# Performance work log

Hardware: AMD Instinct MI355X
Metric: run time of the kernel (lower is better)

Reference implementation:

```python
import jax, jax.numpy as jnp
import numpy as np
import math

D_MODEL = 1024
N_HEADS = 16
D_K = D_MODEL // N_HEADS
B, T = 4, 2048


def setup_inputs() -> dict:
    key = jax.random.key(0)
    k1, k2, k3, k4, k5 = jax.random.split(key, 5)
    s = 1.0 / math.sqrt(D_MODEL)
    return {
        "x": jax.random.normal(k1, (B, T, D_MODEL), dtype=jnp.float32),
        "W_qkv": jax.random.normal(k2, (D_MODEL, 3 * D_MODEL), dtype=jnp.float32) * s,
        "b_qkv": jax.random.normal(k3, (3 * D_MODEL,), dtype=jnp.float32) * 0.02,
        "W_proj": jax.random.normal(k4, (D_MODEL, D_MODEL), dtype=jnp.float32) * s,
        "b_proj": jax.random.normal(k5, (D_MODEL,), dtype=jnp.float32) * 0.02,
    }


def reference(x, W_qkv, b_qkv, W_proj, b_proj):
    Bsz, Tlen, C = x.shape
    qkv = x @ W_qkv + b_qkv                       # [B,T,3C]
    q, k, v = jnp.split(qkv, 3, axis=2)
    # [B,T,C] -> [B,H,T,dk]
    def heads(t):
        return t.reshape(Bsz, Tlen, N_HEADS, D_K).transpose(0, 2, 1, 3)
    q, k, v = heads(q), heads(k), heads(v)
    att = jnp.einsum("bhqd,bhkd->bhqk", q, k) * (1.0 / math.sqrt(D_K))
    causal = jnp.tril(jnp.ones((Tlen, Tlen), dtype=bool))
    att = jnp.where(causal, att, -jnp.inf)
    att = jax.nn.softmax(att, axis=-1)
    y = jnp.einsum("bhqk,bhkd->bhqd", att, v)     # [B,H,T,dk]
    y = y.transpose(0, 2, 1, 3).reshape(Bsz, Tlen, C)
    return y @ W_proj + b_proj
```

## Files before the change

### kernel.cpp

```cpp
#include <hip/hip_runtime.h>
#include <math.h>
#include <stdint.h>

#define D_MODEL 1024
#define NH      16
#define DK      64
#define BS      4
#define TS      2048
#define M_ROWS  (BS*TS)
#define C3      (3*D_MODEL)

typedef __attribute__((ext_vector_type(8))) short          short8;
typedef __attribute__((ext_vector_type(4))) float          f32x4;
typedef __attribute__((ext_vector_type(8))) __bf16         bf16x8;
typedef __attribute__((ext_vector_type(4))) unsigned short ushort4_t;

static __device__ __forceinline__ unsigned short f2bf(float f) {
    unsigned u = __builtin_bit_cast(unsigned, f);
    u += 0x7fffu + ((u >> 16) & 1u);
    return (unsigned short)(u >> 16);
}
static __device__ __forceinline__ float bf2f(unsigned short h) {
    unsigned u = ((unsigned)h) << 16;
    return __builtin_bit_cast(float, u);
}
static __device__ __forceinline__ f32x4 mfma16(short8 a, short8 b, f32x4 c) {
    return __builtin_amdgcn_mfma_f32_16x16x32_bf16(
        __builtin_bit_cast(bf16x8, a), __builtin_bit_cast(bf16x8, b), c, 0, 0, 0);
}
static __device__ __forceinline__ void gll16(const void* g, void* l) {
    __builtin_amdgcn_global_load_lds(
        (const __attribute__((address_space(1))) void*)g,
        (__attribute__((address_space(3))) void*)l, 16, 0, 0);
}

__global__ __launch_bounds__(256)
void cast_split(const float* __restrict__ src, unsigned short* __restrict__ hi,
                unsigned short* __restrict__ lo, int n4) {
    int i = blockIdx.x * blockDim.x + threadIdx.x;
    const int stride = gridDim.x * blockDim.x;
    for (; i < n4; i += stride) {
        float4 v = reinterpret_cast<const float4*>(src)[i];
        float f0 = v.x, f1 = v.y, f2 = v.z, f3 = v.w;
        ushort4_t h, l;
        h[0] = f2bf(f0); l[0] = f2bf(f0 - bf2f(h[0]));
        h[1] = f2bf(f1); l[1] = f2bf(f1 - bf2f(h[1]));
        h[2] = f2bf(f2); l[2] = f2bf(f2 - bf2f(h[2]));
        h[3] = f2bf(f3); l[3] = f2bf(f3 - bf2f(h[3]));
        reinterpret_cast<ushort4_t*>(hi)[i] = h;
        reinterpret_cast<ushort4_t*>(lo)[i] = l;
    }
}

__global__ __launch_bounds__(256)
void cast_wT(const float* __restrict__ W, unsigned short* __restrict__ Th,
             unsigned short* __restrict__ Tl, int K, int N) {
    __shared__ float Ls[32][36];
    const int tid = threadIdx.x;
    const int n0 = blockIdx.x * 32, k0 = blockIdx.y * 32;
    {
        const int row = tid >> 3, c4 = tid & 7;
        float4 v = *reinterpret_cast<const float4*>(&W[(size_t)(k0 + row) * N + n0 + c4 * 4]);
        *reinterpret_cast<float4*>(&Ls[row][c4 * 4]) = v;
    }
    __syncthreads();
    {
        const int nl = tid >> 3, c4 = tid & 7;
        ushort4_t h, l;
#pragma unroll
        for (int j = 0; j < 4; ++j) {
            float f = Ls[c4 * 4 + j][nl];
            h[j] = f2bf(f);
            l[j] = f2bf(f - bf2f(h[j]));
        }
        const size_t o = (size_t)(n0 + nl) * K + k0 + c4 * 4;
        *reinterpret_cast<ushort4_t*>(&Th[o]) = h;
        *reinterpret_cast<ushort4_t*>(&Tl[o]) = l;
    }
}

__global__ __launch_bounds__(256)
void v_transpose(const unsigned short* __restrict__ qh, const unsigned short* __restrict__ ql,
                 unsigned short* __restrict__ vth, unsigned short* __restrict__ vtl) {
    __shared__ unsigned short Ls[64][68];
    const int tt = blockIdx.x, bh = blockIdx.y;
    const int b = bh >> 4, h = bh & 15;
    const size_t src_base = ((size_t)b * TS + (size_t)tt * 64) * C3 + 2 * D_MODEL + h * DK;
    const size_t dst_base = (size_t)bh * DK * TS + (size_t)tt * 64;
#pragma unroll
    for (int pass = 0; pass < 2; ++pass) {
        const unsigned short* src = pass ? ql : qh;
        unsigned short* dst = pass ? vtl : vth;
        if (pass) __syncthreads();
        for (int c = threadIdx.x; c < 1024; c += 256) {
            const int t = c >> 4, c4 = c & 15;
            ushort4_t v = *reinterpret_cast<const ushort4_t*>(&src[src_base + (size_t)t * C3 + c4 * 4]);
            *reinterpret_cast<ushort4_t*>(&Ls[t][c4 * 4]) = v;
        }
        __syncthreads();
        for (int c = threadIdx.x; c < 1024; c += 256) {
            const int d = c >> 4, t4 = c & 15;
            ushort4_t o;
            o[0] = Ls[t4 * 4 + 0][d];
            o[1] = Ls[t4 * 4 + 1][d];
            o[2] = Ls[t4 * 4 + 2][d];
            o[3] = Ls[t4 * 4 + 3][d];
            *reinterpret_cast<ushort4_t*>(&dst[dst_base + (size_t)d * TS + t4 * 4]) = o;
        }
    }
}

template <int BF16OUT>
__global__ __launch_bounds__(256)
void gemm_split(const unsigned short* __restrict__ Ah_g, const unsigned short* __restrict__ Al_g,
                const unsigned short* __restrict__ Bh_g, const unsigned short* __restrict__ Bl_g,
                const float* __restrict__ bias,
                float* __restrict__ Cf, unsigned short* __restrict__ Ch,
                unsigned short* __restrict__ Cl,
                int M, int N, int K) {
    __shared__ unsigned short AhL[128 * 32];
    __shared__ unsigned short AlL[128 * 32];
    __shared__ unsigned short BhL[128 * 32];
    __shared__ unsigned short BlL[128 * 32];

    const int tid  = threadIdx.x;
    const int lane = tid & 63, wid = tid >> 6;
    const int wm = wid >> 1, wn = wid & 1;
    const int bm = blockIdx.y * 128, bn = blockIdx.x * 128;
    const int lr = lane & 15, kg = lane >> 4;

    f32x4 acc[4][4];
#pragma unroll
    for (int m = 0; m < 4; ++m)
#pragma unroll
        for (int n = 0; n < 4; ++n) acc[m][n] = (f32x4){0.f, 0.f, 0.f, 0.f};

    for (int k0 = 0; k0 < K; k0 += 32) {
        __syncthreads();
#pragma unroll
        for (int j = 0; j < 2; ++j) {
            const int si  = j * 256 + wid * 64 + lane;
            const int row = si >> 2, cc = si & 3;
            const int sc  = cc ^ ((row >> 1) & 3);
            const int lo  = (j * 256 + wid * 64) * 8;
            const size_t ga = (size_t)(bm + row) * K + k0 + sc * 8;
            const size_t gb = (size_t)(bn + row) * K + k0 + sc * 8;
            gll16(&Ah_g[ga], &AhL[lo]);
            gll16(&Al_g[ga], &AlL[lo]);
            gll16(&Bh_g[gb], &BhL[lo]);
            gll16(&Bl_g[gb], &BlL[lo]);
        }
        __syncthreads();

        short8 ah[4], al[4], bh[4], bl[4];
#pragma unroll
        for (int m = 0; m < 4; ++m) {
            const int r = wm * 64 + m * 16 + lr;
            const int s = kg ^ ((r >> 1) & 3);
            ah[m] = *reinterpret_cast<const short8*>(&AhL[r * 32 + s * 8]);
            al[m] = *reinterpret_cast<const short8*>(&AlL[r * 32 + s * 8]);
        }
#pragma unroll
        for (int n = 0; n < 4; ++n) {
            const int r = wn * 64 + n * 16 + lr;
            const int s = kg ^ ((r >> 1) & 3);
            bh[n] = *reinterpret_cast<const short8*>(&BhL[r * 32 + s * 8]);
            bl[n] = *reinterpret_cast<const short8*>(&BlL[r * 32 + s * 8]);
        }
#pragma unroll
        for (int m = 0; m < 4; ++m)
#pragma unroll
            for (int n = 0; n < 4; ++n) {
                acc[m][n] = mfma16(ah[m], bh[n], acc[m][n]);
                acc[m][n] = mfma16(ah[m], bl[n], acc[m][n]);
                acc[m][n] = mfma16(al[m], bh[n], acc[m][n]);
            }
    }

    const int og = lane >> 4, oc = lane & 15;
#pragma unroll
    for (int n = 0; n < 4; ++n) {
        const int gc = bn + wn * 64 + n * 16 + oc;
        const float bz = bias[gc];
#pragma unroll
        for (int m = 0; m < 4; ++m) {
            const int gr0 = bm + wm * 64 + m * 16 + og * 4;
#pragma unroll
            for (int rr = 0; rr < 4; ++rr) {
                const float v = acc[m][n][rr] + bz;
                const size_t idx = (size_t)(gr0 + rr) * N + gc;
                if (BF16OUT) {
                    const unsigned short hh = f2bf(v);
                    Ch[idx] = hh;
                    Cl[idx] = f2bf(v - bf2f(hh));
                } else {
                    Cf[idx] = v;
                }
            }
        }
    }
}

__global__ __launch_bounds__(512, 2)
void attn_mfma(const unsigned short* __restrict__ qkvh,
               const unsigned short* __restrict__ vth, const unsigned short* __restrict__ vtl,
               unsigned short* __restrict__ yh, unsigned short* __restrict__ yl) {
    const int pr = blockIdx.x;
    const int bh = blockIdx.y;
    const int b = bh >> 4, h = bh & 15;
    const int tid = threadIdx.x, w = tid >> 6, lane = tid & 63;
    const int lr = lane & 15, lg = lane >> 4;

    __shared__ unsigned short Kt[2][64 * 64];
    __shared__ unsigned short Vhs[2][64 * 64];
    __shared__ unsigned short Vls[2][64 * 64];
    __shared__ unsigned short Ps[8][32 * 64];

    const size_t kbase  = (size_t)b * TS * C3 + D_MODEL + (size_t)h * DK;
    const size_t vbase  = (size_t)bh * DK * TS;
    const size_t qbase  = (size_t)b * TS * C3 + (size_t)h * DK;
    unsigned short* PsW = &Ps[w][0];

    const f32x4 fz = (f32x4){0.f, 0.f, 0.f, 0.f};

    const int srow = tid >> 3;
    const int ssc  = (tid & 7) ^ (srow & 7);
    const int slds = (w * 64) * 8;

    for (int qi = 0; qi < 2; ++qi) {
        const int qt = qi ? (7 - pr) : pr;
        const int q0 = qt * 256;
        const int qwbase = q0 + w * 32;

        short8 qreg[2][2];
#pragma unroll
        for (int mf = 0; mf < 2; ++mf) {
            const size_t qrow = qbase + (size_t)(qwbase + mf * 16 + lr) * C3;
            qreg[mf][0] = *reinterpret_cast<const short8*>(&qkvh[qrow + lg * 8]);
            qreg[mf][1] = *reinterpret_cast<const short8*>(&qkvh[qrow + 32 + lg * 8]);
        }

        f32x4 yacc[4][2];
#pragma unroll
        for (int df = 0; df < 4; ++df)
#pragma unroll
            for (int qf = 0; qf < 2; ++qf) yacc[df][qf] = fz;
        float mrun[2], lrun[2];
#pragma unroll
        for (int qf = 0; qf < 2; ++qf) { mrun[qf] = -1e30f; lrun[qf] = 0.f; }

        const int nkt = 4 * qt + 4;
        int cur = 0;

        auto stage = [&](int buf, int kt) {
            gll16(&qkvh[kbase + (size_t)(kt * 64 + srow) * C3 + ssc * 8], &Kt[buf][slds]);
            gll16(&vth[vbase + (size_t)srow * TS + kt * 64 + ssc * 8], &Vhs[buf][slds]);
            gll16(&vtl[vbase + (size_t)srow * TS + kt * 64 + ssc * 8], &Vls[buf][slds]);
        };
        auto ldsf = [&](const unsigned short* Tt, int row, int kslot) -> short8 {
            return *reinterpret_cast<const short8*>(
                reinterpret_cast<const char*>(Tt) + row * 128 + (((kslot ^ (row & 7)) & 7) << 4));
        };

        stage(cur, 0);
        for (int kt = 0; kt < nkt; ++kt) {
            __syncthreads();
            if (kt + 1 < nkt) stage(cur ^ 1, kt + 1);

            if (kt * 64 <= qwbase + 31) {
                f32x4 s[2][4];
                __builtin_amdgcn_s_setprio(1);
#pragma unroll
                for (int nf = 0; nf < 4; ++nf) {
                    const int krow = nf * 16 + lr;
                    short8 ka0 = ldsf(Kt[cur], krow, lg);
                    short8 ka1 = ldsf(Kt[cur], krow, 4 + lg);
#pragma unroll
                    for (int mf = 0; mf < 2; ++mf)
                        s[mf][nf] = mfma16(ka1, qreg[mf][1], mfma16(ka0, qreg[mf][0], fz));
                }
                __builtin_amdgcn_s_setprio(0);
#pragma unroll
                for (int mf = 0; mf < 2; ++mf)
#pragma unroll
                    for (int nf = 0; nf < 4; ++nf) s[mf][nf] *= 0.125f;
                if (kt * 64 + 63 > qwbase) {
#pragma unroll
                    for (int mf = 0; mf < 2; ++mf) {
                        const int q = qwbase + mf * 16 + lr;
#pragma unroll
                        for (int nf = 0; nf < 4; ++nf)
#pragma unroll
                            for (int rr = 0; rr < 4; ++rr)
                                if (kt * 64 + nf * 16 + lg * 4 + rr > q) s[mf][nf][rr] = -1e30f;
                    }
                }
                float sclv[2];
#pragma unroll
                for (int mf = 0; mf < 2; ++mf) {
                    float rm = s[mf][0][0];
#pragma unroll
                    for (int nf = 0; nf < 4; ++nf)
#pragma unroll
                        for (int rr = 0; rr < 4; ++rr) rm = fmaxf(rm, s[mf][nf][rr]);
                    rm = fmaxf(rm, __shfl_xor(rm, 16, 64));
                    rm = fmaxf(rm, __shfl_xor(rm, 32, 64));
                    const float mn = fmaxf(mrun[mf], rm);
                    float rs = 0.f;
#pragma unroll
                    for (int nf = 0; nf < 4; ++nf)
#pragma unroll
                        for (int rr = 0; rr < 4; ++rr) {
                            const float p = __expf(s[mf][nf][rr] - mn);
                            s[mf][nf][rr] = p;
                            rs += p;
                        }
                    rs += __shfl_xor(rs, 16, 64);
                    rs += __shfl_xor(rs, 32, 64);
                    sclv[mf] = __expf(mrun[mf] - mn);
                    lrun[mf] = lrun[mf] * sclv[mf] + rs;
                    mrun[mf] = mn;
                }
#pragma unroll
                for (int df = 0; df < 4; ++df)
#pragma unroll
                    for (int qf = 0; qf < 2; ++qf) yacc[df][qf] *= sclv[qf];
#pragma unroll
                for (int mf = 0; mf < 2; ++mf) {
                    const int q = mf * 16 + lr;
#pragma unroll
                    for (int nf = 0; nf < 4; ++nf) {
                        ushort4_t pw;
                        pw[0] = f2bf(s[mf][nf][0]);
                        pw[1] = f2bf(s[mf][nf][1]);
                        pw[2] = f2bf(s[mf][nf][2]);
                        pw[3] = f2bf(s[mf][nf][3]);
                        *reinterpret_cast<ushort4_t*>(
                            reinterpret_cast<char*>(PsW) +
                            ((q * 128 + (nf * 16 + lg * 4) * 2) ^ ((q & 7) << 4))) = pw;
                    }
                }
#pragma unroll
                for (int kf = 0; kf < 2; ++kf) {
                    short8 pb[2];
#pragma unroll
                    for (int qf = 0; qf < 2; ++qf) {
                        const int q = qf * 16 + lr;
                        pb[qf] = *reinterpret_cast<const short8*>(
                            reinterpret_cast<const char*>(PsW) +
                            q * 128 + ((((kf << 2) + lg) ^ (q & 7)) << 4));
                    }
                    __builtin_amdgcn_s_setprio(1);
#pragma unroll
                    for (int df = 0; df < 4; ++df) {
                        const int d = df * 16 + lr;
                        short8 va = ldsf(Vhs[cur], d, (kf << 2) + lg);
                        short8 vb = ldsf(Vls[cur], d, (kf << 2) + lg);
#pragma unroll
                        for (int qf = 0; qf < 2; ++qf) {
                            yacc[df][qf] = mfma16(va, pb[qf], yacc[df][qf]);
                            yacc[df][qf] = mfma16(vb, pb[qf], yacc[df][qf]);
                        }
                    }
                    __builtin_amdgcn_s_setprio(0);
                }
            }
            cur ^= 1;
        }

#pragma unroll
        for (int qf = 0; qf < 2; ++qf) {
            const float inv = 1.f / lrun[qf];
            const size_t ro = ((size_t)b * TS + (qwbase + qf * 16 + lr)) * D_MODEL + h * DK;
#pragma unroll
            for (int df = 0; df < 4; ++df) {
                ushort4_t oh, ol;
#pragma unroll
                for (int rr = 0; rr < 4; ++rr) {
                    const float v = yacc[df][qf][rr] * inv;
                    oh[rr] = f2bf(v);
                    ol[rr] = f2bf(v - bf2f(oh[rr]));
                }
                *reinterpret_cast<ushort4_t*>(&yh[ro + df * 16 + lg * 4]) = oh;
                *reinterpret_cast<ushort4_t*>(&yl[ro + df * 16 + lg * 4]) = ol;
            }
        }
    }
}

extern "C" void kernel_launch(void* const* d_in, const int* in_sizes, int n_in,
                              void* d_out, int out_size, void* d_ws, size_t ws_size,
                              hipStream_t stream) {
    const float* x      = (const float*)d_in[0];
    const float* W_qkv  = (const float*)d_in[1];
    const float* b_qkv  = (const float*)d_in[2];
    const float* W_proj = (const float*)d_in[3];
    const float* b_proj = (const float*)d_in[4];
    float* out = (float*)d_out;

    char* ws = (char*)d_ws;
    size_t off = 0;
    auto carve = [&](size_t elems) {
        unsigned short* p = (unsigned short*)(ws + off);
        off += elems * sizeof(unsigned short);
        return p;
    };
    unsigned short* xh   = carve((size_t)M_ROWS * D_MODEL);
    unsigned short* xl   = carve((size_t)M_ROWS * D_MODEL);
    unsigned short* wqh  = carve((size_t)C3 * D_MODEL);
    unsigned short* wql  = carve((size_t)C3 * D_MODEL);
    unsigned short* wph  = carve((size_t)D_MODEL * D_MODEL);
    unsigned short* wpl  = carve((size_t)D_MODEL * D_MODEL);
    unsigned short* qkvh = carve((size_t)M_ROWS * C3);
    unsigned short* qkvl = carve((size_t)M_ROWS * C3);
    unsigned short* vth  = carve((size_t)BS * NH * DK * TS);
    unsigned short* vtl  = carve((size_t)BS * NH * DK * TS);
    unsigned short* yhh  = carve((size_t)M_ROWS * D_MODEL);
    unsigned short* yll  = carve((size_t)M_ROWS * D_MODEL);

    cast_split<<<2048, 256, 0, stream>>>(x, xh, xl, M_ROWS * D_MODEL / 4);
    cast_wT<<<dim3(C3 / 32, D_MODEL / 32), 256, 0, stream>>>(W_qkv, wqh, wql, D_MODEL, C3);
    cast_wT<<<dim3(D_MODEL / 32, D_MODEL / 32), 256, 0, stream>>>(W_proj, wph, wpl, D_MODEL, D_MODEL);

    gemm_split<1><<<dim3(C3 / 128, M_ROWS / 128), 256, 0, stream>>>(
        xh, xl, wqh, wql, b_qkv, nullptr, qkvh, qkvl, M_ROWS, C3, D_MODEL);

    v_transpose<<<dim3(TS / 64, BS * NH), 256, 0, stream>>>(qkvh, qkvl, vth, vtl);

    attn_mfma<<<dim3(4, BS * NH), 512, 0, stream>>>(qkvh, vth, vtl, yhh, yll);

    gemm_split<0><<<dim3(D_MODEL / 128, M_ROWS / 128), 256, 0, stream>>>(
        yhh, yll, wph, wpl, b_proj, out, nullptr, nullptr, M_ROWS, D_MODEL, D_MODEL);
}
```

Baseline: 451.8 us.

## Rewrite split-bf16 GEMM as 256x128 triple-buffered 8-wave pipelined kernel

Replaces the 128x128, 4-wave split-bf16 GEMM with a 256x128 tile run by 8 waves. The three hi/lo product terms are folded into a single virtual K axis of length 3K. Global-to-LDS loads go into a three-stage ring buffer with explicit vmcnt waits, barriers and s_setprio, so loads for tile t+2 overlap the MFMAs for tile t. The goal is to hide memory latency and cut per-iteration synchronisation. In exchange it uses more LDS (one block per CU), adds complex index math, and makes correctness depend on the hand-placed waitcnt and barrier schedule.

```diff
diff --git a/kernel.cpp b/kernel.cpp
--- a/kernel.cpp
+++ b/kernel.cpp
@@ -111,23 +111,22 @@
 }
 
 template <int BF16OUT>
-__global__ __launch_bounds__(256)
-void gemm_split(const unsigned short* __restrict__ Ah_g, const unsigned short* __restrict__ Al_g,
-                const unsigned short* __restrict__ Bh_g, const unsigned short* __restrict__ Bl_g,
-                const float* __restrict__ bias,
-                float* __restrict__ Cf, unsigned short* __restrict__ Ch,
-                unsigned short* __restrict__ Cl,
-                int M, int N, int K) {
-    __shared__ unsigned short AhL[128 * 32];
-    __shared__ unsigned short AlL[128 * 32];
-    __shared__ unsigned short BhL[128 * 32];
-    __shared__ unsigned short BlL[128 * 32];
+__global__ __launch_bounds__(512, 1)
+void gemm_split_8ph(const unsigned short* __restrict__ Ah_g, const unsigned short* __restrict__ Al_g,
+                    const unsigned short* __restrict__ Bh_g, const unsigned short* __restrict__ Bl_g,
+                    const float* __restrict__ bias,
+                    float* __restrict__ Cf, unsigned short* __restrict__ Ch,
+                    unsigned short* __restrict__ Cl,
+                    int M, int N, int K) {
+    __shared__ unsigned short ALs[3][256 * 64];
+    __shared__ unsigned short BLs[3][128 * 64];
 
     const int tid  = threadIdx.x;
     const int lane = tid & 63, wid = tid >> 6;
     const int wm = wid >> 1, wn = wid & 1;
-    const int bm = blockIdx.y * 128, bn = blockIdx.x * 128;
+    const int bm = blockIdx.y * 256, bn = blockIdx.x * 128;
     const int lr = lane & 15, kg = lane >> 4;
+    const int NT = (3 * K) / 64;
 
     f32x4 acc[4][4];
 #pragma unroll
@@ -135,46 +134,102 @@
 #pragma unroll
         for (int n = 0; n < 4; ++n) acc[m][n] = (f32x4){0.f, 0.f, 0.f, 0.f};
 
-    for (int k0 = 0; k0 < K; k0 += 32) {
-        __syncthreads();
+    auto stageA = [&](int t) {
+        const int b3 = t % 3;
+#pragma unroll
+        for (int half = 0; half < 2; ++half)
+#pragma unroll
+            for (int j = 0; j < 2; ++j) {
+                const int L   = (wid * 2 + j) * 64 + lane;
+                const int row = L >> 3, sl = L & 7;
+                const int sv  = sl ^ (row & 7);
+                const int vc  = t * 2 + (sv >> 2);
+                const int r3  = vc % 3;
+                const int c   = vc / 3;
+                const unsigned short* pl = (r3 == 2) ? Al_g : Ah_g;
+                const size_t ga = (size_t)(bm + half * 128 + row) * K + c * 32 + (sv & 3) * 8;
+                gll16(&pl[ga], &ALs[b3][half * 8192 + (wid * 2 + j) * 512]);
+            }
+    };
+    auto stageB = [&](int t) {
+        const int b3 = t % 3;
 #pragma unroll
         for (int j = 0; j < 2; ++j) {
-            const int si  = j * 256 + wid * 64 + lane;
-            const int row = si >> 2, cc = si & 3;
-            const int sc  = cc ^ ((row >> 1) & 3);
-            const int lo  = (j * 256 + wid * 64) * 8;
-            const size_t ga = (size_t)(bm + row) * K + k0 + sc * 8;
-            const size_t gb = (size_t)(bn + row) * K + k0 + sc * 8;
-            gll16(&Ah_g[ga], &AhL[lo]);
-            gll16(&Al_g[ga], &AlL[lo]);
-            gll16(&Bh_g[gb], &BhL[lo]);
-            gll16(&Bl_g[gb], &BlL[lo]);
-        }
-        __syncthreads();
-
-        short8 ah[4], al[4], bh[4], bl[4];
-#pragma unroll
-        for (int m = 0; m < 4; ++m) {
-            const int r = wm * 64 + m * 16 + lr;
-            const int s = kg ^ ((r >> 1) & 3);
-            ah[m] = *reinterpret_cast<const short8*>(&AhL[r * 32 + s * 8]);
-            al[m] = *reinterpret_cast<const short8*>(&AlL[r * 32 + s * 8]);
-        }
+            const int L   = (wid * 2 + j) * 64 + lane;
+            const int row = L >> 3, sl = L & 7;
+            const int sv  = sl ^ (row & 7);
+            const int vc  = t * 2 + (sv >> 2);
+            const int r3  = vc % 3;
+            const int c   = vc / 3;
+            const unsigned short* pl = (r3 == 1) ? Bl_g : Bh_g;
+            const size_t gb = (size_t)(bn + row) * K + c * 32 + (sv & 3) * 8;
+            gll16(&pl[gb], &BLs[b3][(wid * 2 + j) * 512]);
+        }
+    };
+    auto rdA = [&](int cur, int m, int kf) -> short8 {
+        const int row = wm * 64 + m * 16 + lr;
+        const int sp  = (kf * 4 + kg) ^ (row & 7);
+        return *reinterpret_cast<const short8*>(&ALs[cur][row * 64 + sp * 8]);
+    };
+    auto rdB = [&](int cur, int n, int kf) -> short8 {
+        const int row = wn * 64 + n * 16 + lr;
+        const int sp  = (kf * 4 + kg) ^ (row & 7);
+        return *reinterpret_cast<const short8*>(&BLs[cur][row * 64 + sp * 8]);
+    };
+
+    stageA(0); stageB(0);
+    stageA(1); stageB(1);
+    asm volatile("s_waitcnt vmcnt(6)" ::: "memory");
+    __builtin_amdgcn_s_barrier();
+
+    for (int t = 0; t < NT; ++t) {
+        const int cur = t % 3;
+        short8 bfr[4][2];
 #pragma unroll
         for (int n = 0; n < 4; ++n) {
-            const int r = wn * 64 + n * 16 + lr;
-            const int s = kg ^ ((r >> 1) & 3);
-            bh[n] = *reinterpret_cast<const short8*>(&BhL[r * 32 + s * 8]);
-            bl[n] = *reinterpret_cast<const short8*>(&BlL[r * 32 + s * 8]);
-        }
-#pragma unroll
-        for (int m = 0; m < 4; ++m)
+            bfr[n][0] = rdB(cur, n, 0);
+            bfr[n][1] = rdB(cur, n, 1);
+        }
+        short8 afr[2][2];
+#pragma unroll
+        for (int m = 0; m < 2; ++m) {
+            afr[m][0] = rdA(cur, m, 0);
+            afr[m][1] = rdA(cur, m, 1);
+        }
+        if (t + 2 < NT) stageA(t + 2);
+        __builtin_amdgcn_s_barrier();
+        __builtin_amdgcn_s_setprio(1);
+#pragma unroll
+        for (int m = 0; m < 2; ++m)
 #pragma unroll
             for (int n = 0; n < 4; ++n) {
-                acc[m][n] = mfma16(ah[m], bh[n], acc[m][n]);
-                acc[m][n] = mfma16(ah[m], bl[n], acc[m][n]);
-                acc[m][n] = mfma16(al[m], bh[n], acc[m][n]);
-            }
+                acc[m][n] = mfma16(afr[m][0], bfr[n][0], acc[m][n]);
+                acc[m][n] = mfma16(afr[m][1], bfr[n][1], acc[m][n]);
+            }
+        __builtin_amdgcn_s_setprio(0);
+        __builtin_amdgcn_s_barrier();
+#pragma unroll
+        for (int m = 0; m < 2; ++m) {
+            afr[m][0] = rdA(cur, m + 2, 0);
+            afr[m][1] = rdA(cur, m + 2, 1);
+        }
+        if (t + 2 < NT) {
+            stageB(t + 2);
+            asm volatile("s_waitcnt vmcnt(6)" ::: "memory");
+        } else if (t + 1 < NT) {
+            asm volatile("s_waitcnt vmcnt(0)" ::: "memory");
+        }
+        __builtin_amdgcn_s_barrier();
+        __builtin_amdgcn_s_setprio(1);
+#pragma unroll
+        for (int m = 0; m < 2; ++m)
+#pragma unroll
+            for (int n = 0; n < 4; ++n) {
+                acc[m + 2][n] = mfma16(afr[m][0], bfr[n][0], acc[m + 2][n]);
+                acc[m + 2][n] = mfma16(afr[m][1], bfr[n][1], acc[m + 2][n]);
+            }
+        __builtin_amdgcn_s_setprio(0);
+        __builtin_amdgcn_s_barrier();
     }
 
     const int og = lane >> 4, oc = lane & 15;
@@ -422,13 +477,13 @@
     cast_wT<<<dim3(C3 / 32, D_MODEL / 32), 256, 0, stream>>>(W_qkv, wqh, wql, D_MODEL, C3);
     cast_wT<<<dim3(D_MODEL / 32, D_MODEL / 32), 256, 0, stream>>>(W_proj, wph, wpl, D_MODEL, D_MODEL);
 
-    gemm_split<1><<<dim3(C3 / 128, M_ROWS / 128), 256, 0, stream>>>(
+    gemm_split_8ph<1><<<dim3(C3 / 128, M_ROWS / 256), 512, 0, stream>>>(
         xh, xl, wqh, wql, b_qkv, nullptr, qkvh, qkvl, M_ROWS, C3, D_MODEL);
 
     v_transpose<<<dim3(TS / 64, BS * NH), 256, 0, stream>>>(qkvh, qkvl, vth, vtl);
 
     attn_mfma<<<dim3(4, BS * NH), 512, 0, stream>>>(qkvh, vth, vtl, yhh, yll);
 
-    gemm_split<0><<<dim3(D_MODEL / 128, M_ROWS / 128), 256, 0, stream>>>(
+    gemm_split_8ph<0><<<dim3(D_MODEL / 128, M_ROWS / 256), 512, 0, stream>>>(
         yhh, yll, wph, wpl, b_proj, out, nullptr, nullptr, M_ROWS, D_MODEL, D_MODEL);
 }
```

Measured after the change: 508.5 us. +12.5%, slower.

## Rewrite split-bf16 GEMM as persistent 256x128 tiles with double-buffered LDS

Applied to the files above, without the earlier changes.

Replaces the 128x128 single-buffered GEMM with a 512-thread kernel that computes 256x128 tiles, launched as exactly 256 blocks, one per CU, each looping over NTILE column tiles. The block index is remapped so blocks sharing A rows group together for L2 reuse. The next K-slice is loaded into a second LDS buffer while the current one feeds the MFMAs, with s_setprio raised around the MFMA section. The aim is to hide global-load latency, halve barriers per K-step and fill the machine evenly, at the cost of more LDS use and one block per CU, which gives less latency hiding across blocks. The tile mapping hard-codes K=1024 (32 steps) and grid dimensions specific to these shapes.

```diff
diff --git a/kernel.cpp b/kernel.cpp
--- a/kernel.cpp
+++ b/kernel.cpp
@@ -110,91 +110,112 @@
     }
 }
 
-template <int BF16OUT>
-__global__ __launch_bounds__(256)
-void gemm_split(const unsigned short* __restrict__ Ah_g, const unsigned short* __restrict__ Al_g,
-                const unsigned short* __restrict__ Bh_g, const unsigned short* __restrict__ Bl_g,
-                const float* __restrict__ bias,
-                float* __restrict__ Cf, unsigned short* __restrict__ Ch,
-                unsigned short* __restrict__ Cl,
-                int M, int N, int K) {
-    __shared__ unsigned short AhL[128 * 32];
-    __shared__ unsigned short AlL[128 * 32];
-    __shared__ unsigned short BhL[128 * 32];
-    __shared__ unsigned short BlL[128 * 32];
+template <int BF16OUT, int NTILE>
+__global__ __launch_bounds__(512, 1)
+void gemm_split2(const unsigned short* __restrict__ Ah_g, const unsigned short* __restrict__ Al_g,
+                 const unsigned short* __restrict__ Bh_g, const unsigned short* __restrict__ Bl_g,
+                 const float* __restrict__ bias,
+                 float* __restrict__ Cf, unsigned short* __restrict__ Ch,
+                 unsigned short* __restrict__ Cl,
+                 int M, int N, int K) {
+    __shared__ unsigned short AhL[2][256 * 32];
+    __shared__ unsigned short AlL[2][256 * 32];
+    __shared__ unsigned short BhL[2][128 * 32];
+    __shared__ unsigned short BlL[2][128 * 32];
 
     const int tid  = threadIdx.x;
     const int lane = tid & 63, wid = tid >> 6;
     const int wm = wid >> 1, wn = wid & 1;
-    const int bm = blockIdx.y * 128, bn = blockIdx.x * 128;
     const int lr = lane & 15, kg = lane >> 4;
 
-    f32x4 acc[4][4];
-#pragma unroll
-    for (int m = 0; m < 4; ++m)
-#pragma unroll
-        for (int n = 0; n < 4; ++n) acc[m][n] = (f32x4){0.f, 0.f, 0.f, 0.f};
-
-    for (int k0 = 0; k0 < K; k0 += 32) {
+    const int bid = blockIdx.x;
+    const int mb  = 4 * (bid & 7) + (bid >> 6);
+    const int ng  = (bid >> 3) & 7;
+    const int bm  = mb * 256;
+
+    const int arow0 = tid >> 2;
+    const int ao0   = (tid & 3) ^ ((arow0 >> 1) & 3);
+    const int arow1 = arow0 + 128;
+    const int ao1   = (tid & 3) ^ ((arow1 >> 1) & 3);
+    const int brow  = tid >> 2;
+    const int bo    = (tid & 3) ^ ((brow >> 1) & 3);
+    const int ldsw  = wid * 512;
+
+    for (int it = 0; it < NTILE; ++it) {
+        const int bn = (ng * NTILE + it) * 128;
+
+        f32x4 acc[4][4];
+#pragma unroll
+        for (int m = 0; m < 4; ++m)
+#pragma unroll
+            for (int n = 0; n < 4; ++n) acc[m][n] = (f32x4){0.f, 0.f, 0.f, 0.f};
+
+        auto stage = [&](int buf, int k0) {
+            gll16(&Ah_g[(size_t)(bm + arow0) * K + k0 + ao0 * 8], &AhL[buf][ldsw]);
+            gll16(&Ah_g[(size_t)(bm + arow1) * K + k0 + ao1 * 8], &AhL[buf][4096 + ldsw]);
+            gll16(&Al_g[(size_t)(bm + arow0) * K + k0 + ao0 * 8], &AlL[buf][ldsw]);
+            gll16(&Al_g[(size_t)(bm + arow1) * K + k0 + ao1 * 8], &AlL[buf][4096 + ldsw]);
+            gll16(&Bh_g[(size_t)(bn + brow) * K + k0 + bo * 8], &BhL[buf][ldsw]);
+            gll16(&Bl_g[(size_t)(bn + brow) * K + k0 + bo * 8], &BlL[buf][ldsw]);
+        };
+        auto rd = [&](const unsigned short* P, int r) -> short8 {
+            const int s = kg ^ ((r >> 1) & 3);
+            return *reinterpret_cast<const short8*>(&P[r * 32 + s * 8]);
+        };
+
+        int cur = 0;
+        stage(0, 0);
         __syncthreads();
-#pragma unroll
-        for (int j = 0; j < 2; ++j) {
-            const int si  = j * 256 + wid * 64 + lane;
-            const int row = si >> 2, cc = si & 3;
-            const int sc  = cc ^ ((row >> 1) & 3);
-            const int lo  = (j * 256 + wid * 64) * 8;
-            const size_t ga = (size_t)(bm + row) * K + k0 + sc * 8;
-            const size_t gb = (size_t)(bn + row) * K + k0 + sc * 8;
-            gll16(&Ah_g[ga], &AhL[lo]);
-            gll16(&Al_g[ga], &AlL[lo]);
-            gll16(&Bh_g[gb], &BhL[lo]);
-            gll16(&Bl_g[gb], &BlL[lo]);
-        }
-        __syncthreads();
-
-        short8 ah[4], al[4], bh[4], bl[4];
-#pragma unroll
-        for (int m = 0; m < 4; ++m) {
-            const int r = wm * 64 + m * 16 + lr;
-            const int s = kg ^ ((r >> 1) & 3);
-            ah[m] = *reinterpret_cast<const short8*>(&AhL[r * 32 + s * 8]);
-            al[m] = *reinterpret_cast<const short8*>(&AlL[r * 32 + s * 8]);
-        }
+
+        for (int t = 0; t < 32; ++t) {
+            if (t + 1 < 32) stage(cur ^ 1, (t + 1) * 32);
+
+            short8 ah[4], al[4], bhf[4], blf[4];
+#pragma unroll
+            for (int m = 0; m < 4; ++m) {
+                const int r = wm * 64 + m * 16 + lr;
+                ah[m] = rd(&AhL[cur][0], r);
+                al[m] = rd(&AlL[cur][0], r);
+            }
+#pragma unroll
+            for (int n = 0; n < 4; ++n) {
+                const int r = wn * 64 + n * 16 + lr;
+                bhf[n] = rd(&BhL[cur][0], r);
+                blf[n] = rd(&BlL[cur][0], r);
+            }
+            __builtin_amdgcn_s_setprio(1);
+#pragma unroll
+            for (int m = 0; m < 4; ++m)
+#pragma unroll
+                for (int n = 0; n < 4; ++n) {
+                    acc[m][n] = mfma16(ah[m], bhf[n], acc[m][n]);
+                    acc[m][n] = mfma16(ah[m], blf[n], acc[m][n]);
+                    acc[m][n] = mfma16(al[m], bhf[n], acc[m][n]);
+                }
+            __builtin_amdgcn_s_setprio(0);
+            __syncthreads();
+            cur ^= 1;
+        }
+
+        const int og = lane >> 4, oc = lane & 15;
 #pragma unroll
         for (int n = 0; n < 4; ++n) {
-            const int r = wn * 64 + n * 16 + lr;
-            const int s = kg ^ ((r >> 1) & 3);
-            bh[n] = *reinterpret_cast<const short8*>(&BhL[r * 32 + s * 8]);
-            bl[n] = *reinterpret_cast<const short8*>(&BlL[r * 32 + s * 8]);
-        }
-#pragma unroll
-        for (int m = 0; m < 4; ++m)
-#pragma unroll
-            for (int n = 0; n < 4; ++n) {
-                acc[m][n] = mfma16(ah[m], bh[n], acc[m][n]);
-                acc[m][n] = mfma16(ah[m], bl[n], acc[m][n]);
-                acc[m][n] = mfma16(al[m], bh[n], acc[m][n]);
-            }
-    }
-
-    const int og = lane >> 4, oc = lane & 15;
-#pragma unroll
-    for (int n = 0; n < 4; ++n) {
-        const int gc = bn + wn * 64 + n * 16 + oc;
-        const float bz = bias[gc];
-#pragma unroll
-        for (int m = 0; m < 4; ++m) {
-            const int gr0 = bm + wm * 64 + m * 16 + og * 4;
-#pragma unroll
-            for (int rr = 0; rr < 4; ++rr) {
-                const float v = acc[m][n][rr] + bz;
-                const size_t idx = (size_t)(gr0 + rr) * N + gc;
-                if (BF16OUT) {
-                    const unsigned short hh = f2bf(v);
-                    Ch[idx] = hh;
-                    Cl[idx] = f2bf(v - bf2f(hh));
-                } else {
-                    Cf[idx] = v;
+            const int gc = bn + wn * 64 + n * 16 + oc;
+            const float bz = bias[gc];
+#pragma unroll
+            for (int m = 0; m < 4; ++m) {
+                const int gr0 = bm + wm * 64 + m * 16 + og * 4;
+#pragma unroll
+                for (int rr = 0; rr < 4; ++rr) {
+                    const float v = acc[m][n][rr] + bz;
+                    const size_t idx = (size_t)(gr0 + rr) * N + gc;
+                    if (BF16OUT) {
+                        const unsigned short hh = f2bf(v);
+                        Ch[idx] = hh;
+                        Cl[idx] = f2bf(v - bf2f(hh));
+                    } else {
+                        Cf[idx] = v;
+                    }
                 }
             }
         }
@@ -422,13 +443,13 @@
     cast_wT<<<dim3(C3 / 32, D_MODEL / 32), 256, 0, stream>>>(W_qkv, wqh, wql, D_MODEL, C3);
     cast_wT<<<dim3(D_MODEL / 32, D_MODEL / 32), 256, 0, stream>>>(W_proj, wph, wpl, D_MODEL, D_MODEL);
 
-    gemm_split<1><<<dim3(C3 / 128, M_ROWS / 128), 256, 0, stream>>>(
+    gemm_split2<1, 3><<<256, 512, 0, stream>>>(
         xh, xl, wqh, wql, b_qkv, nullptr, qkvh, qkvl, M_ROWS, C3, D_MODEL);
 
     v_transpose<<<dim3(TS / 64, BS * NH), 256, 0, stream>>>(qkvh, qkvl, vth, vtl);
 
     attn_mfma<<<dim3(4, BS * NH), 512, 0, stream>>>(qkvh, vth, vtl, yhh, yll);
 
-    gemm_split<0><<<dim3(D_MODEL / 128, M_ROWS / 128), 256, 0, stream>>>(
+    gemm_split2<0, 1><<<256, 512, 0, stream>>>(
         yhh, yll, wph, wpl, b_proj, out, nullptr, nullptr, M_ROWS, D_MODEL, D_MODEL);
 }
```

Measured after the change: 458.5 us. About the same (+1.5%).

## Fuse V transpose into QKV GEMM epilogue and give each attention block one query tile

Applied to the files above, without the earlier changes.

The QKV GEMM epilogue now writes the V columns straight into the transposed hi/lo V buffers, so the separate v_transpose kernel and its extra read/write pass over V are gone. The attention kernel no longer pairs a short and a long causal query tile per block. It launches 8 blocks per head, each handling one query tile, which doubles the grid but leaves blocks with uneven causal work. The transposed V stores are 4-element ushort4 writes strided by the sequence length, which may coalesce less well than the old transpose kernel's writes.

```diff
diff --git a/kernel.cpp b/kernel.cpp
--- a/kernel.cpp
+++ b/kernel.cpp
@@ -79,44 +79,14 @@
     }
 }
 
-__global__ __launch_bounds__(256)
-void v_transpose(const unsigned short* __restrict__ qh, const unsigned short* __restrict__ ql,
-                 unsigned short* __restrict__ vth, unsigned short* __restrict__ vtl) {
-    __shared__ unsigned short Ls[64][68];
-    const int tt = blockIdx.x, bh = blockIdx.y;
-    const int b = bh >> 4, h = bh & 15;
-    const size_t src_base = ((size_t)b * TS + (size_t)tt * 64) * C3 + 2 * D_MODEL + h * DK;
-    const size_t dst_base = (size_t)bh * DK * TS + (size_t)tt * 64;
-#pragma unroll
-    for (int pass = 0; pass < 2; ++pass) {
-        const unsigned short* src = pass ? ql : qh;
-        unsigned short* dst = pass ? vtl : vth;
-        if (pass) __syncthreads();
-        for (int c = threadIdx.x; c < 1024; c += 256) {
-            const int t = c >> 4, c4 = c & 15;
-            ushort4_t v = *reinterpret_cast<const ushort4_t*>(&src[src_base + (size_t)t * C3 + c4 * 4]);
-            *reinterpret_cast<ushort4_t*>(&Ls[t][c4 * 4]) = v;
-        }
-        __syncthreads();
-        for (int c = threadIdx.x; c < 1024; c += 256) {
-            const int d = c >> 4, t4 = c & 15;
-            ushort4_t o;
-            o[0] = Ls[t4 * 4 + 0][d];
-            o[1] = Ls[t4 * 4 + 1][d];
-            o[2] = Ls[t4 * 4 + 2][d];
-            o[3] = Ls[t4 * 4 + 3][d];
-            *reinterpret_cast<ushort4_t*>(&dst[dst_base + (size_t)d * TS + t4 * 4]) = o;
-        }
-    }
-}
-
-template <int BF16OUT>
+template <int MODE>
 __global__ __launch_bounds__(256)
 void gemm_split(const unsigned short* __restrict__ Ah_g, const unsigned short* __restrict__ Al_g,
                 const unsigned short* __restrict__ Bh_g, const unsigned short* __restrict__ Bl_g,
                 const float* __restrict__ bias,
                 float* __restrict__ Cf, unsigned short* __restrict__ Ch,
                 unsigned short* __restrict__ Cl,
+                unsigned short* __restrict__ vth, unsigned short* __restrict__ vtl,
                 int M, int N, int K) {
     __shared__ unsigned short AhL[128 * 32];
     __shared__ unsigned short AlL[128 * 32];
@@ -178,23 +148,48 @@
     }
 
     const int og = lane >> 4, oc = lane & 15;
-#pragma unroll
-    for (int n = 0; n < 4; ++n) {
-        const int gc = bn + wn * 64 + n * 16 + oc;
-        const float bz = bias[gc];
-#pragma unroll
-        for (int m = 0; m < 4; ++m) {
-            const int gr0 = bm + wm * 64 + m * 16 + og * 4;
-#pragma unroll
-            for (int rr = 0; rr < 4; ++rr) {
-                const float v = acc[m][n][rr] + bz;
-                const size_t idx = (size_t)(gr0 + rr) * N + gc;
-                if (BF16OUT) {
-                    const unsigned short hh = f2bf(v);
-                    Ch[idx] = hh;
-                    Cl[idx] = f2bf(v - bf2f(hh));
-                } else {
-                    Cf[idx] = v;
+    if (MODE == 2 && bn >= 2048) {
+#pragma unroll
+        for (int n = 0; n < 4; ++n) {
+            const int gc = bn + wn * 64 + n * 16 + oc;
+            const float bz = bias[gc];
+            const int vb  = gc - 2048;
+            const int hh_ = vb >> 6, dd = vb & 63;
+#pragma unroll
+            for (int m = 0; m < 4; ++m) {
+                const int gr0 = bm + wm * 64 + m * 16 + og * 4;
+                ushort4_t vh4, vl4;
+#pragma unroll
+                for (int rr = 0; rr < 4; ++rr) {
+                    const float v = acc[m][n][rr] + bz;
+                    vh4[rr] = f2bf(v);
+                    vl4[rr] = f2bf(v - bf2f(vh4[rr]));
+                }
+                const size_t o = ((size_t)((gr0 >> 11) * 16 + hh_) * 64 + dd) * 2048
+                               + (size_t)(gr0 & 2047);
+                *reinterpret_cast<ushort4_t*>(&vth[o]) = vh4;
+                *reinterpret_cast<ushort4_t*>(&vtl[o]) = vl4;
+            }
+        }
+    } else {
+#pragma unroll
+        for (int n = 0; n < 4; ++n) {
+            const int gc = bn + wn * 64 + n * 16 + oc;
+            const float bz = bias[gc];
+#pragma unroll
+            for (int m = 0; m < 4; ++m) {
+                const int gr0 = bm + wm * 64 + m * 16 + og * 4;
+#pragma unroll
+                for (int rr = 0; rr < 4; ++rr) {
+                    const float v = acc[m][n][rr] + bz;
+                    const size_t idx = (size_t)(gr0 + rr) * N + gc;
+                    if (MODE >= 1) {
+                        const unsigned short hh = f2bf(v);
+                        Ch[idx] = hh;
+                        Cl[idx] = f2bf(v - bf2f(hh));
+                    } else {
+                        Cf[idx] = v;
+                    }
                 }
             }
         }
@@ -205,7 +200,7 @@
 void attn_mfma(const unsigned short* __restrict__ qkvh,
                const unsigned short* __restrict__ vth, const unsigned short* __restrict__ vtl,
                unsigned short* __restrict__ yh, unsigned short* __restrict__ yl) {
-    const int pr = blockIdx.x;
+    const int qt = blockIdx.x;
     const int bh = blockIdx.y;
     const int b = bh >> 4, h = bh & 15;
     const int tid = threadIdx.x, w = tid >> 6, lane = tid & 63;
@@ -227,163 +222,159 @@
     const int ssc  = (tid & 7) ^ (srow & 7);
     const int slds = (w * 64) * 8;
 
-    for (int qi = 0; qi < 2; ++qi) {
-        const int qt = qi ? (7 - pr) : pr;
-        const int q0 = qt * 256;
-        const int qwbase = q0 + w * 32;
-
-        short8 qreg[2][2];
-#pragma unroll
-        for (int mf = 0; mf < 2; ++mf) {
-            const size_t qrow = qbase + (size_t)(qwbase + mf * 16 + lr) * C3;
-            qreg[mf][0] = *reinterpret_cast<const short8*>(&qkvh[qrow + lg * 8]);
-            qreg[mf][1] = *reinterpret_cast<const short8*>(&qkvh[qrow + 32 + lg * 8]);
-        }
-
-        f32x4 yacc[4][2];
-#pragma unroll
-        for (int df = 0; df < 4; ++df)
-#pragma unroll
-            for (int qf = 0; qf < 2; ++qf) yacc[df][qf] = fz;
-        float mrun[2], lrun[2];
-#pragma unroll
-        for (int qf = 0; qf < 2; ++qf) { mrun[qf] = -1e30f; lrun[qf] = 0.f; }
-
-        const int nkt = 4 * qt + 4;
-        int cur = 0;
-
-        auto stage = [&](int buf, int kt) {
-            gll16(&qkvh[kbase + (size_t)(kt * 64 + srow) * C3 + ssc * 8], &Kt[buf][slds]);
-            gll16(&vth[vbase + (size_t)srow * TS + kt * 64 + ssc * 8], &Vhs[buf][slds]);
-            gll16(&vtl[vbase + (size_t)srow * TS + kt * 64 + ssc * 8], &Vls[buf][slds]);
-        };
-        auto ldsf = [&](const unsigned short* Tt, int row, int kslot) -> short8 {
-            return *reinterpret_cast<const short8*>(
-                reinterpret_cast<const char*>(Tt) + row * 128 + (((kslot ^ (row & 7)) & 7) << 4));
-        };
-
-        stage(cur, 0);
-        for (int kt = 0; kt < nkt; ++kt) {
-            __syncthreads();
-            if (kt + 1 < nkt) stage(cur ^ 1, kt + 1);
-
-            if (kt * 64 <= qwbase + 31) {
-                f32x4 s[2][4];
+    const int qwbase = qt * 256 + w * 32;
+
+    short8 qreg[2][2];
+#pragma unroll
+    for (int mf = 0; mf < 2; ++mf) {
+        const size_t qrow = qbase + (size_t)(qwbase + mf * 16 + lr) * C3;
+        qreg[mf][0] = *reinterpret_cast<const short8*>(&qkvh[qrow + lg * 8]);
+        qreg[mf][1] = *reinterpret_cast<const short8*>(&qkvh[qrow + 32 + lg * 8]);
+    }
+
+    f32x4 yacc[4][2];
+#pragma unroll
+    for (int df = 0; df < 4; ++df)
+#pragma unroll
+        for (int qf = 0; qf < 2; ++qf) yacc[df][qf] = fz;
+    float mrun[2], lrun[2];
+#pragma unroll
+    for (int qf = 0; qf < 2; ++qf) { mrun[qf] = -1e30f; lrun[qf] = 0.f; }
+
+    const int nkt = 4 * qt + 4;
+    int cur = 0;
+
+    auto stage = [&](int buf, int kt) {
+        gll16(&qkvh[kbase + (size_t)(kt * 64 + srow) * C3 + ssc * 8], &Kt[buf][slds]);
+        gll16(&vth[vbase + (size_t)srow * TS + kt * 64 + ssc * 8], &Vhs[buf][slds]);
+        gll16(&vtl[vbase + (size_t)srow * TS + kt * 64 + ssc * 8], &Vls[buf][slds]);
+    };
+    auto ldsf = [&](const unsigned short* Tt, int row, int kslot) -> short8 {
+        return *reinterpret_cast<const short8*>(
+            reinterpret_cast<const char*>(Tt) + row * 128 + (((kslot ^ (row & 7)) & 7) << 4));
+    };
+
+    stage(cur, 0);
+    for (int kt = 0; kt < nkt; ++kt) {
+        __syncthreads();
+        if (kt + 1 < nkt) stage(cur ^ 1, kt + 1);
+
+        if (kt * 64 <= qwbase + 31) {
+            f32x4 s[2][4];
+            __builtin_amdgcn_s_setprio(1);
+#pragma unroll
+            for (int nf = 0; nf < 4; ++nf) {
+                const int krow = nf * 16 + lr;
+                short8 ka0 = ldsf(Kt[cur], krow, lg);
+                short8 ka1 = ldsf(Kt[cur], krow, 4 + lg);
+#pragma unroll
+                for (int mf = 0; mf < 2; ++mf)
+                    s[mf][nf] = mfma16(ka1, qreg[mf][1], mfma16(ka0, qreg[mf][0], fz));
+            }
+            __builtin_amdgcn_s_setprio(0);
+#pragma unroll
+            for (int mf = 0; mf < 2; ++mf)
+#pragma unroll
+                for (int nf = 0; nf < 4; ++nf) s[mf][nf] *= 0.125f;
+            if (kt * 64 + 63 > qwbase) {
+#pragma unroll
+                for (int mf = 0; mf < 2; ++mf) {
+                    const int q = qwbase + mf * 16 + lr;
+#pragma unroll
+                    for (int nf = 0; nf < 4; ++nf)
+#pragma unroll
+                        for (int rr = 0; rr < 4; ++rr)
+                            if (kt * 64 + nf * 16 + lg * 4 + rr > q) s[mf][nf][rr] = -1e30f;
+                }
+            }
+            float sclv[2];
+#pragma unroll
+            for (int mf = 0; mf < 2; ++mf) {
+                float rm = s[mf][0][0];
+#pragma unroll
+                for (int nf = 0; nf < 4; ++nf)
+#pragma unroll
+                    for (int rr = 0; rr < 4; ++rr) rm = fmaxf(rm, s[mf][nf][rr]);
+                rm = fmaxf(rm, __shfl_xor(rm, 16, 64));
+                rm = fmaxf(rm, __shfl_xor(rm, 32, 64));
+                const float mn = fmaxf(mrun[mf], rm);
+                float rs = 0.f;
+#pragma unroll
+                for (int nf = 0; nf < 4; ++nf)
+#pragma unroll
+                    for (int rr = 0; rr < 4; ++rr) {
+                        const float p = __expf(s[mf][nf][rr] - mn);
+                        s[mf][nf][rr] = p;
+                        rs += p;
+                    }
+                rs += __shfl_xor(rs, 16, 64);
+                rs += __shfl_xor(rs, 32, 64);
+                sclv[mf] = __expf(mrun[mf] - mn);
+                lrun[mf] = lrun[mf] * sclv[mf] + rs;
+                mrun[mf] = mn;
+            }
+#pragma unroll
+            for (int df = 0; df < 4; ++df)
+#pragma unroll
+                for (int qf = 0; qf < 2; ++qf) yacc[df][qf] *= sclv[qf];
+#pragma unroll
+            for (int mf = 0; mf < 2; ++mf) {
+                const int q = mf * 16 + lr;
+#pragma unroll
+                for (int nf = 0; nf < 4; ++nf) {
+                    ushort4_t pw;
+                    pw[0] = f2bf(s[mf][nf][0]);
+                    pw[1] = f2bf(s[mf][nf][1]);
+                    pw[2] = f2bf(s[mf][nf][2]);
+                    pw[3] = f2bf(s[mf][nf][3]);
+                    *reinterpret_cast<ushort4_t*>(
+                        reinterpret_cast<char*>(PsW) +
+                        ((q * 128 + (nf * 16 + lg * 4) * 2) ^ ((q & 7) << 4))) = pw;
+                }
+            }
+#pragma unroll
+            for (int kf = 0; kf < 2; ++kf) {
+                short8 pb[2];
+#pragma unroll
+                for (int qf = 0; qf < 2; ++qf) {
+                    const int q = qf * 16 + lr;
+                    pb[qf] = *reinterpret_cast<const short8*>(
+                        reinterpret_cast<const char*>(PsW) +
+                        q * 128 + ((((kf << 2) + lg) ^ (q & 7)) << 4));
+                }
                 __builtin_amdgcn_s_setprio(1);
 #pragma unroll
-                for (int nf = 0; nf < 4; ++nf) {
-                    const int krow = nf * 16 + lr;
-                    short8 ka0 = ldsf(Kt[cur], krow, lg);
-                    short8 ka1 = ldsf(Kt[cur], krow, 4 + lg);
-#pragma unroll
-                    for (int mf = 0; mf < 2; ++mf)
-                        s[mf][nf] = mfma16(ka1, qreg[mf][1], mfma16(ka0, qreg[mf][0], fz));
+                for (int df = 0; df < 4; ++df) {
+                    const int d = df * 16 + lr;
+                    short8 va = ldsf(Vhs[cur], d, (kf << 2) + lg);
+                    short8 vb = ldsf(Vls[cur], d, (kf << 2) + lg);
+#pragma unroll
+                    for (int qf = 0; qf < 2; ++qf) {
+                        yacc[df][qf] = mfma16(va, pb[qf], yacc[df][qf]);
+                        yacc[df][qf] = mfma16(vb, pb[qf], yacc[df][qf]);
+                    }
                 }
                 __builtin_amdgcn_s_setprio(0);
-#pragma unroll
-                for (int mf = 0; mf < 2; ++mf)
-#pragma unroll
-                    for (int nf = 0; nf < 4; ++nf) s[mf][nf] *= 0.125f;
-                if (kt * 64 + 63 > qwbase) {
-#pragma unroll
-                    for (int mf = 0; mf < 2; ++mf) {
-                        const int q = qwbase + mf * 16 + lr;
-#pragma unroll
-                        for (int nf = 0; nf < 4; ++nf)
-#pragma unroll
-                            for (int rr = 0; rr < 4; ++rr)
-                                if (kt * 64 + nf * 16 + lg * 4 + rr > q) s[mf][nf][rr] = -1e30f;
-                    }
-                }
-                float sclv[2];
-#pragma unroll
-                for (int mf = 0; mf < 2; ++mf) {
-                    float rm = s[mf][0][0];
-#pragma unroll
-                    for (int nf = 0; nf < 4; ++nf)
-#pragma unroll
-                        for (int rr = 0; rr < 4; ++rr) rm = fmaxf(rm, s[mf][nf][rr]);
-                    rm = fmaxf(rm, __shfl_xor(rm, 16, 64));
-                    rm = fmaxf(rm, __shfl_xor(rm, 32, 64));
-                    const float mn = fmaxf(mrun[mf], rm);
-                    float rs = 0.f;
-#pragma unroll
-                    for (int nf = 0; nf < 4; ++nf)
-#pragma unroll
-                        for (int rr = 0; rr < 4; ++rr) {
-                            const float p = __expf(s[mf][nf][rr] - mn);
-                            s[mf][nf][rr] = p;
-                            rs += p;
-                        }
-                    rs += __shfl_xor(rs, 16, 64);
-                    rs += __shfl_xor(rs, 32, 64);
-                    sclv[mf] = __expf(mrun[mf] - mn);
-                    lrun[mf] = lrun[mf] * sclv[mf] + rs;
-                    mrun[mf] = mn;
-                }
-#pragma unroll
-                for (int df = 0; df < 4; ++df)
-#pragma unroll
-                    for (int qf = 0; qf < 2; ++qf) yacc[df][qf] *= sclv[qf];
-#pragma unroll
-                for (int mf = 0; mf < 2; ++mf) {
-                    const int q = mf * 16 + lr;
-#pragma unroll
-                    for (int nf = 0; nf < 4; ++nf) {
-                        ushort4_t pw;
-                        pw[0] = f2bf(s[mf][nf][0]);
-                        pw[1] = f2bf(s[mf][nf][1]);
-                        pw[2] = f2bf(s[mf][nf][2]);
-                        pw[3] = f2bf(s[mf][nf][3]);
-                        *reinterpret_cast<ushort4_t*>(
-                            reinterpret_cast<char*>(PsW) +
-                            ((q * 128 + (nf * 16 + lg * 4) * 2) ^ ((q & 7) << 4))) = pw;
-                    }
-                }
-#pragma unroll
-                for (int kf = 0; kf < 2; ++kf) {
-                    short8 pb[2];
-#pragma unroll
-                    for (int qf = 0; qf < 2; ++qf) {
-                        const int q = qf * 16 + lr;
-                        pb[qf] = *reinterpret_cast<const short8*>(
-                            reinterpret_cast<const char*>(PsW) +
-                            q * 128 + ((((kf << 2) + lg) ^ (q & 7)) << 4));
-                    }
-                    __builtin_amdgcn_s_setprio(1);
-#pragma unroll
-                    for (int df = 0; df < 4; ++df) {
-                        const int d = df * 16 + lr;
-                        short8 va = ldsf(Vhs[cur], d, (kf << 2) + lg);
-                        short8 vb = ldsf(Vls[cur], d, (kf << 2) + lg);
-#pragma unroll
-                        for (int qf = 0; qf < 2; ++qf) {
-                            yacc[df][qf] = mfma16(va, pb[qf], yacc[df][qf]);
-                            yacc[df][qf] = mfma16(vb, pb[qf], yacc[df][qf]);
-                        }
-                    }
-                    __builtin_amdgcn_s_setprio(0);
-                }
-            }
-            cur ^= 1;
-        }
-
-#pragma unroll
-        for (int qf = 0; qf < 2; ++qf) {
-            const float inv = 1.f / lrun[qf];
-            const size_t ro = ((size_t)b * TS + (qwbase + qf * 16 + lr)) * D_MODEL + h * DK;
-#pragma unroll
-            for (int df = 0; df < 4; ++df) {
-                ushort4_t oh, ol;
-#pragma unroll
-                for (int rr = 0; rr < 4; ++rr) {
-                    const float v = yacc[df][qf][rr] * inv;
-                    oh[rr] = f2bf(v);
-                    ol[rr] = f2bf(v - bf2f(oh[rr]));
-                }
-                *reinterpret_cast<ushort4_t*>(&yh[ro + df * 16 + lg * 4]) = oh;
-                *reinterpret_cast<ushort4_t*>(&yl[ro + df * 16 + lg * 4]) = ol;
-            }
+            }
+        }
+        cur ^= 1;
+    }
+
+#pragma unroll
+    for (int qf = 0; qf < 2; ++qf) {
+        const float inv = 1.f / lrun[qf];
+        const size_t ro = ((size_t)b * TS + (qwbase + qf * 16 + lr)) * D_MODEL + h * DK;
+#pragma unroll
+        for (int df = 0; df < 4; ++df) {
+            ushort4_t oh, ol;
+#pragma unroll
+            for (int rr = 0; rr < 4; ++rr) {
+                const float v = yacc[df][qf][rr] * inv;
+                oh[rr] = f2bf(v);
+                ol[rr] = f2bf(v - bf2f(oh[rr]));
+            }
+            *reinterpret_cast<ushort4_t*>(&yh[ro + df * 16 + lg * 4]) = oh;
+            *reinterpret_cast<ushort4_t*>(&yl[ro + df * 16 + lg * 4]) = ol;
         }
     }
 }
@@ -422,13 +413,12 @@
     cast_wT<<<dim3(C3 / 32, D_MODEL / 32), 256, 0, stream>>>(W_qkv, wqh, wql, D_MODEL, C3);
     cast_wT<<<dim3(D_MODEL / 32, D_MODEL / 32), 256, 0, stream>>>(W_proj, wph, wpl, D_MODEL, D_MODEL);
 
-    gemm_split<1><<<dim3(C3 / 128, M_ROWS / 128), 256, 0, stream>>>(
-        xh, xl, wqh, wql, b_qkv, nullptr, qkvh, qkvl, M_ROWS, C3, D_MODEL);
-
-    v_transpose<<<dim3(TS / 64, BS * NH), 256, 0, stream>>>(qkvh, qkvl, vth, vtl);
-
-    attn_mfma<<<dim3(4, BS * NH), 512, 0, stream>>>(qkvh, vth, vtl, yhh, yll);
+    gemm_split<2><<<dim3(C3 / 128, M_ROWS / 128), 256, 0, stream>>>(
+        xh, xl, wqh, wql, b_qkv, nullptr, qkvh, qkvl, vth, vtl, M_ROWS, C3, D_MODEL);
+
+    attn_mfma<<<dim3(8, BS * NH), 512, 0, stream>>>(qkvh, vth, vtl, yhh, yll);
 
     gemm_split<0><<<dim3(D_MODEL / 128, M_ROWS / 128), 256, 0, stream>>>(
-        yhh, yll, wph, wpl, b_proj, out, nullptr, nullptr, M_ROWS, D_MODEL, D_MODEL);
-}
+        yhh, yll, wph, wpl, b_proj, out, nullptr, nullptr, nullptr, nullptr,
+        M_ROWS, D_MODEL, D_MODEL);
+}
```

After: 498.2 us. 10.3% more time.
